# Kernel optimization log

Measured on AMD Instinct MI355X. Metric: run time of the kernel, lower is better.

The kernel has to match this reference:

```python
import jax, jax.numpy as jnp
import numpy as np

N, D = 8192, 1024  # tokens, model dim (d == D required by residual add)


def setup_inputs() -> dict:
    key = jax.random.key(0)
    ks = jax.random.split(key, 6)
    s = 1.0 / np.sqrt(D)
    return {
        "x": jax.random.normal(ks[0], (N, D), dtype=jnp.float32),
        "Wq": jax.random.normal(ks[1], (D, D), dtype=jnp.float32) * s,
        "Wk": jax.random.normal(ks[2], (D, D), dtype=jnp.float32) * s,
        "Wg": jax.random.normal(ks[3], (D, D), dtype=jnp.float32) * s,
        "Wm_w": jax.random.normal(ks[4], (D, 1), dtype=jnp.float32) * s,
        "Wm_b": jnp.zeros((1,), dtype=jnp.float32),
        "c": jnp.asarray(1.0 / np.sqrt(D), dtype=jnp.float32),
    }


def reference(x, Wq, Wk, Wg, Wm_w, Wm_b, c):
    # projections [N, d]
    q_hat = x @ Wq
    k_hat = x @ Wk
    # mean-center over the token axis
    q = q_hat - jnp.mean(q_hat, axis=0, keepdims=True)
    k = k_hat - jnp.mean(k_hat, axis=0, keepdims=True)
    # scaled scores [N, N], row softmax
    attn = jax.nn.softmax(c * (q @ k.T), axis=-1)
    # per-token gate m [N, 1], softmax over tokens, broadcast over columns
    m = x @ Wm_w + Wm_b
    gate = jax.nn.softmax(m, axis=0)
    omega = attn + gate  # [N, N]
    g = x @ Wg           # [N, d]
    return omega @ g + x  # residual, requires d == D
```

## Files before the change

kernel.cpp:

```cpp
#include <hip/hip_runtime.h>
#include <math.h>


#define NT 8192
#define DD 1024

typedef float v4f __attribute__((ext_vector_type(4)));
typedef short v8s __attribute__((ext_vector_type(8)));
typedef int   v4i __attribute__((ext_vector_type(4)));
typedef int   v8i __attribute__((ext_vector_type(8)));

typedef const __attribute__((address_space(1))) void* gp_t;
typedef __attribute__((address_space(3))) void* lp_t;

__device__ __forceinline__ short f2b(float f) {
    unsigned u = __float_as_uint(f);
    return (short)((u + 0x7fffu + ((u >> 16) & 1u)) >> 16);
}
__device__ __forceinline__ char f2e4m3(float f) {
    unsigned p = __builtin_amdgcn_cvt_pk_fp8_f32(f, f, 0, false);
    return (char)(p & 0xff);
}

__device__ __forceinline__ void tile_coords(int bid, int tn, int& bm, int& bn) {
    const int SUP = 16;
    int per = SUP * tn;
    int band = bid / per, r = bid % per;
    bm = band * SUP + (r % SUP);
    bn = r / SUP;
}

__device__ __forceinline__ void gemm_core_fp8(const char* __restrict__ A,
                                              const char* __restrict__ B,
                                              int K, int m0, int n0,
                                              char* smem, v4f (&acc)[4][4])
{
    char* lsA = smem;
    char* lsB = smem + 16384;
    const int tid  = threadIdx.x;
    const int wave = tid >> 6, lane = tid & 63;
    const int l15 = lane & 15, l4 = lane >> 4;
    const int wm = (wave >> 1) << 6, wn = (wave & 1) << 6;

#pragma unroll
    for (int i = 0; i < 4; i++)
#pragma unroll
        for (int j = 0; j < 4; j++) acc[i][j] = (v4f)(0.0f);

    const int srow = lane >> 3;
    const int g    = (lane & 7) ^ srow;

    for (int k0 = 0; k0 < K; k0 += 128) {
#pragma unroll
        for (int i = 0; i < 4; i++) {
            int ci  = wave * 4 + i;
            int row = ci * 8 + srow;
            const char* ga = A + (size_t)(m0 + row) * K + k0 + g * 16;
            const char* gb = B + (size_t)(n0 + row) * K + k0 + g * 16;
            __builtin_amdgcn_global_load_lds((gp_t)ga, (lp_t)(lsA + ci * 1024), 16, 0, 0);
            __builtin_amdgcn_global_load_lds((gp_t)gb, (lp_t)(lsB + ci * 1024), 16, 0, 0);
        }
        __syncthreads();
#pragma unroll
        for (int kk = 0; kk < 128; kk += 32) {
            long af[4], bq[4];
            const int cbase = (kk >> 4) + (l4 >> 1);
            const int half  = (l4 & 1) * 8;
#pragma unroll
            for (int t = 0; t < 4; t++) {
                int ra = wm + t * 16 + l15;
                int ca = cbase ^ (ra & 7);
                af[t] = *(const long*)(lsA + ra * 128 + ca * 16 + half);
                int rb = wn + t * 16 + l15;
                int cb = cbase ^ (rb & 7);
                bq[t] = *(const long*)(lsB + rb * 128 + cb * 16 + half);
            }
#pragma unroll
            for (int i = 0; i < 4; i++)
#pragma unroll
                for (int j = 0; j < 4; j++)
                    acc[i][j] = __builtin_amdgcn_mfma_f32_16x16x32_fp8_fp8(af[i], bq[j], acc[i][j], 0, 0, 0);
        }
        __syncthreads();
    }
}

__device__ __forceinline__ void gemm_core_mx(const char* __restrict__ A,
                                             const char* __restrict__ B,
                                             int K, int m0, int n0,
                                             char* smem, v4f (&acc)[4][4])
{
    char* lsA = smem;
    char* lsB = smem + 16384;
    const int tid  = threadIdx.x;
    const int wave = tid >> 6, lane = tid & 63;
    const int l15 = lane & 15, l4 = lane >> 4;
    const int wm = (wave >> 1) << 6, wn = (wave & 1) << 6;

#pragma unroll
    for (int i = 0; i < 4; i++)
#pragma unroll
        for (int j = 0; j < 4; j++) acc[i][j] = (v4f)(0.0f);

    const int srow = lane >> 3;
    const int g    = (lane & 7) ^ srow;

    for (int k0 = 0; k0 < K; k0 += 128) {
#pragma unroll
        for (int i = 0; i < 4; i++) {
            int ci  = wave * 4 + i;
            int row = ci * 8 + srow;
            const char* ga = A + (size_t)(m0 + row) * K + k0 + g * 16;
            const char* gb = B + (size_t)(n0 + row) * K + k0 + g * 16;
            __builtin_amdgcn_global_load_lds((gp_t)ga, (lp_t)(lsA + ci * 1024), 16, 0, 0);
            __builtin_amdgcn_global_load_lds((gp_t)gb, (lp_t)(lsB + ci * 1024), 16, 0, 0);
        }
        __syncthreads();
        v8i af[4], bq[4];
#pragma unroll
        for (int t = 0; t < 4; t++) {
            int ra = wm + t * 16 + l15;
            int a0 = (2 * l4) ^ (ra & 7), a1 = (2 * l4 + 1) ^ (ra & 7);
            v4i lo = *(const v4i*)(lsA + ra * 128 + a0 * 16);
            v4i hi = *(const v4i*)(lsA + ra * 128 + a1 * 16);
            af[t][0] = lo[0]; af[t][1] = lo[1]; af[t][2] = lo[2]; af[t][3] = lo[3];
            af[t][4] = hi[0]; af[t][5] = hi[1]; af[t][6] = hi[2]; af[t][7] = hi[3];
            int rb = wn + t * 16 + l15;
            int b0 = (2 * l4) ^ (rb & 7), b1 = (2 * l4 + 1) ^ (rb & 7);
            v4i blo = *(const v4i*)(lsB + rb * 128 + b0 * 16);
            v4i bhi = *(const v4i*)(lsB + rb * 128 + b1 * 16);
            bq[t][0] = blo[0]; bq[t][1] = blo[1]; bq[t][2] = blo[2]; bq[t][3] = blo[3];
            bq[t][4] = bhi[0]; bq[t][5] = bhi[1]; bq[t][6] = bhi[2]; bq[t][7] = bhi[3];
        }
#pragma unroll
        for (int i = 0; i < 4; i++)
#pragma unroll
            for (int j = 0; j < 4; j++)
                acc[i][j] = __builtin_amdgcn_mfma_scale_f32_16x16x128_f8f6f4(
                    af[i], bq[j], acc[i][j], 0, 0,
                    0, 0x7f7f7f7f, 0, 0x7f7f7f7f);
        __syncthreads();
    }
}

__global__ void prep(const float* __restrict__ x, const float* __restrict__ wv,
                     const float* __restrict__ bp, char* __restrict__ x8,
                     float* __restrict__ em,
                     const float* __restrict__ Wq, const float* __restrict__ Wk,
                     const float* __restrict__ Wg, char* __restrict__ w8t,
                     float* __restrict__ zero_base) {
    __shared__ float t[64][68];
    int bid = blockIdx.x, tid = threadIdx.x;
    if (bid < 2048) {
        if (bid == 0) {
            for (int i = tid; i < 2 * DD + NT; i += 256) zero_base[i] = 0.f;
        }
        int wv_id = tid >> 6;
        int row = bid * 4 + wv_id;
        int lane = tid & 63;
        const float* xr = x + (size_t)row * DD;
        char* x8r = x8 + (size_t)row * DD;
        float s = 0.f;
        for (int c = lane * 4; c < DD; c += 256) {
            float4 a = *(const float4*)(xr + c);
            float4 b = *(const float4*)(wv + c);
            s = fmaf(a.x, b.x, s); s = fmaf(a.y, b.y, s);
            s = fmaf(a.z, b.z, s); s = fmaf(a.w, b.w, s);
            unsigned p = __builtin_amdgcn_cvt_pk_fp8_f32(a.x, a.y, 0, false);
            p = __builtin_amdgcn_cvt_pk_fp8_f32(a.z, a.w, p, true);
            *(int*)(x8r + c) = (int)p;
        }
        for (int o = 32; o; o >>= 1) s += __shfl_down(s, o);
        if (lane == 0) em[row] = __expf(s + bp[0]);
    } else {
        int idx = bid - 2048;
        int bz = idx >> 8, rem = idx & 255;
        const float* W = bz == 0 ? Wq : (bz == 1 ? Wk : Wg);
        int k0 = (rem & 15) * 64, n0 = (rem >> 4) * 64;
        int tr = tid >> 4, tc = tid & 15;
#pragma unroll
        for (int p = 0; p < 4; p++) {
            int r = p * 16 + tr;
            float4 v = *(const float4*)(W + (size_t)(k0 + r) * DD + n0 + tc * 4);
            t[r][tc * 4 + 0] = v.x; t[r][tc * 4 + 1] = v.y;
            t[r][tc * 4 + 2] = v.z; t[r][tc * 4 + 3] = v.w;
        }
        __syncthreads();
#pragma unroll
        for (int p = 0; p < 4; p++) {
            int rr = p * 16 + tr;
            unsigned pk = __builtin_amdgcn_cvt_pk_fp8_f32(
                16.f * t[tc * 4 + 0][rr], 16.f * t[tc * 4 + 1][rr], 0, false);
            pk = __builtin_amdgcn_cvt_pk_fp8_f32(
                16.f * t[tc * 4 + 2][rr], 16.f * t[tc * 4 + 3][rr], pk, true);
            *(int*)(w8t + (size_t)(bz * DD + n0 + rr) * DD + k0 + tc * 4) = (int)pk;
        }
    }
}

__global__ void beta_gemv(const char* __restrict__ k8, const float* __restrict__ qsum,
                          const float* __restrict__ cp, float* __restrict__ beta,
                          const float* __restrict__ em, float* __restrict__ gden) {
    int tid = threadIdx.x, lane = tid & 63;
    if (blockIdx.x == 2048) {
        __shared__ float sr[4];
        float s = 0.f;
        for (int i = tid; i < NT; i += 256) s += em[i];
        for (int o = 32; o; o >>= 1) s += __shfl_xor(s, o);
        if (lane == 0) sr[tid >> 6] = s;
        __syncthreads();
        if (tid == 0) gden[0] = sr[0] + sr[1] + sr[2] + sr[3];
        return;
    }
    int row = blockIdx.x * 4 + (tid >> 6);
    v4i kv = *(const v4i*)(k8 + (size_t)row * DD + lane * 16);
    const float* qs = qsum + lane * 16;
    float s = 0.f;
#pragma unroll
    for (int w = 0; w < 4; w++) {
        float4 qv = *(const float4*)(qs + w * 4);
        int word = kv[w];
        s = fmaf(__builtin_amdgcn_cvt_f32_fp8(word, 0), qv.x, s);
        s = fmaf(__builtin_amdgcn_cvt_f32_fp8(word, 1), qv.y, s);
        s = fmaf(__builtin_amdgcn_cvt_f32_fp8(word, 2), qv.z, s);
        s = fmaf(__builtin_amdgcn_cvt_f32_fp8(word, 3), qv.w, s);
    }
    for (int o = 32; o; o >>= 1) s += __shfl_down(s, o);
    if (lane == 0) beta[row] = s * cp[0] / (float)NT;
}


__global__ __launch_bounds__(256, 2) void k_proj(
        const char* __restrict__ x8, const char* __restrict__ w8t,
        char* __restrict__ q8, char* __restrict__ k8, char* __restrict__ gbt,
        float* __restrict__ qsum, float* __restrict__ gsum) {
    __shared__ __align__(16) char smem[32768];
    int bm, bn; tile_coords(blockIdx.x, 24, bm, bn);
    int m0 = bm * 128, n0 = bn * 128;
    v4f acc[4][4];
    gemm_core_fp8(x8, w8t, DD, m0, n0, smem, acc);

    const int tid = threadIdx.x, wave = tid >> 6, lane = tid & 63;
    const int l15 = lane & 15, l4 = lane >> 4;
    const int wm = (wave >> 1) << 6, wn = (wave & 1) << 6;
    int sec = n0 >> 10;
    int nloc = n0 & (DD - 1);
    const float WS = 0.0625f;

    if (sec < 2) {
        char* dst = sec ? k8 : q8;
        float cs[4] = {0.f, 0.f, 0.f, 0.f};
#pragma unroll
        for (int i = 0; i < 4; i++)
#pragma unroll
            for (int j = 0; j < 4; j++)
#pragma unroll
                for (int v = 0; v < 4; v++) {
                    int row = m0 + wm + i * 16 + l4 * 4 + v;
                    int col = nloc + wn + j * 16 + l15;
                    float av = acc[i][j][v] * WS;
                    dst[(size_t)row * DD + col] = f2e4m3(av);
                    cs[j] += av;
                }
        if (sec == 0)
#pragma unroll
            for (int j = 0; j < 4; j++)
                atomicAdd(&qsum[nloc + wn + j * 16 + l15], cs[j]);
    } else {
        char* sc = smem;
        float cs[4] = {0.f, 0.f, 0.f, 0.f};
#pragma unroll
        for (int i = 0; i < 4; i++)
#pragma unroll
            for (int j = 0; j < 4; j++)
#pragma unroll
                for (int v = 0; v < 4; v++) {
                    int lr = wn + j * 16 + l15;
                    int lc = wm + i * 16 + l4 * 4 + v;
                    float av = acc[i][j][v] * WS;
                    sc[lr * 144 + lc] = f2e4m3(av);
                    cs[j] += av;
                }
        __syncthreads();
#pragma unroll
        for (int it = 0; it < 4; it++) {
            int c = it * 256 + tid;
            int dr = c >> 3, cm = (c & 7) * 16;
            int4 vv = *(const int4*)(sc + dr * 144 + cm);
            *(int4*)(gbt + (size_t)(nloc + dr) * NT + m0 + cm) = vv;
        }
#pragma unroll
        for (int j = 0; j < 4; j++)
            atomicAdd(&gsum[nloc + wn + j * 16 + l15], cs[j]);
    }
}

__global__ __launch_bounds__(256, 2) void k_score(
        const char* __restrict__ q8, const char* __restrict__ k8,
        char* __restrict__ E, float* __restrict__ l, const float* __restrict__ cptr,
        const float* __restrict__ beta) {
    __shared__ __align__(16) char smem[32768];
    int bm, bn; tile_coords(blockIdx.x, 64, bm, bn);
    int m0 = bm * 128, n0 = bn * 128;
    v4f acc[4][4];
    gemm_core_fp8(q8, k8, DD, m0, n0, smem, acc);

    const float cv = cptr[0];
    const int tid = threadIdx.x, wave = tid >> 6, lane = tid & 63;
    const int l15 = lane & 15, l4 = lane >> 4;
    const int wm = (wave >> 1) << 6, wn = (wave & 1) << 6;
    float bj[4];
#pragma unroll
    for (int j = 0; j < 4; j++) bj[j] = beta[n0 + wn + j * 16 + l15];
#pragma unroll
    for (int i = 0; i < 4; i++)
#pragma unroll
        for (int v = 0; v < 4; v++) {
            int row = m0 + wm + i * 16 + l4 * 4 + v;
            float rsum = 0.f;
#pragma unroll
            for (int j = 0; j < 4; j++) {
                float e = __expf(cv * acc[i][j][v] - bj[j]);
                E[(size_t)row * NT + (n0 + wn + j * 16 + l15)] = f2e4m3(e);
                rsum += e;
            }
#pragma unroll
            for (int o = 1; o < 16; o <<= 1) rsum += __shfl_xor(rsum, o);
            if (l15 == 0) atomicAdd(&l[row], rsum);
        }
}

__global__ __launch_bounds__(256, 2) void k_out(
        const char* __restrict__ E, const char* __restrict__ gbt,
        const float* __restrict__ l, const float* __restrict__ em,
        const float* __restrict__ gden, const float* __restrict__ gsum,
        const float* __restrict__ x, float* __restrict__ out) {
    __shared__ __align__(16) char smem[32768];
    int bm, bn; tile_coords(blockIdx.x, 8, bm, bn);
    int m0 = bm * 128, n0 = bn * 128;
    v4f acc[4][4];
    gemm_core_mx(E, gbt, NT, m0, n0, smem, acc);

    const float ginv = 1.f / gden[0];
    const int tid = threadIdx.x, wave = tid >> 6, lane = tid & 63;
    const int l15 = lane & 15, l4 = lane >> 4;
    const int wm = (wave >> 1) << 6, wn = (wave & 1) << 6;
#pragma unroll
    for (int i = 0; i < 4; i++)
#pragma unroll
        for (int v = 0; v < 4; v++) {
            int row = m0 + wm + i * 16 + l4 * 4 + v;
            float inv = 1.f / l[row];
            float gv  = em[row] * ginv;
#pragma unroll
            for (int j = 0; j < 4; j++) {
                int col = n0 + wn + j * 16 + l15;
                out[(size_t)row * DD + col] =
                    acc[i][j][v] * inv + gv * gsum[col] + x[(size_t)row * DD + col];
            }
        }
}


extern "C" void kernel_launch(void* const* d_in, const int* in_sizes, int n_in,
                              void* d_out, int out_size, void* d_ws, size_t ws_size,
                              hipStream_t stream) {
    const float* x  = (const float*)d_in[0];
    const float* Wq = (const float*)d_in[1];
    const float* Wk = (const float*)d_in[2];
    const float* Wg = (const float*)d_in[3];
    const float* Wm = (const float*)d_in[4];
    const float* Wb = (const float*)d_in[5];
    const float* cp = (const float*)d_in[6];
    float* out = (float*)d_out;

    char* w = (char*)d_ws;
    size_t off = 0;
    auto alloc = [&](size_t bytes) -> void* {
        void* p = w + off;
        off += (bytes + 255) & ~(size_t)255;
        return p;
    };
    char*  q8    = (char*)alloc((size_t)NT * DD);
    char*  k8    = (char*)alloc((size_t)NT * DD);
    char*  gbt   = (char*)alloc((size_t)DD * NT);
    char*  w8t   = (char*)alloc((size_t)3 * DD * DD);
    char*  x8    = (char*)alloc((size_t)NT * DD);
    char*  E     = (char*)alloc((size_t)NT * NT);
    float* stats = (float*)alloc((2 * DD + 3 * NT + 1) * 4);
    float* qsum = stats;
    float* gsum = stats + DD;
    float* lrow = stats + 2 * DD;
    float* gden = lrow + NT;
    float* em   = gden + 1;
    float* beta = em + NT;
    if (off > ws_size) return;

    prep<<<2048 + 768, 256, 0, stream>>>(x, Wm, Wb, x8, em, Wq, Wk, Wg, w8t, stats);
    k_proj<<<64 * 24, 256, 0, stream>>>(x8, w8t, q8, k8, gbt, qsum, gsum);
    beta_gemv<<<2049, 256, 0, stream>>>(k8, qsum, cp, beta, em, gden);
    k_score<<<64 * 64, 256, 0, stream>>>(q8, k8, E, lrow, cp, beta);
    k_out<<<64 * 8, 256, 0, stream>>>(E, gbt, lrow, em, gden, gsum, x, out);
}
```

Measured before the change: 370.3 us.

## Permute fp8 K-layout so GEMM core uses 16-byte LDS fragment reads

Producers of fp8 operands (x8, transposed weights, q8/k8 outputs and qsum) now write columns in a permuted order within each 128-wide K block. The fp8 GEMM core can then load two MFMA K-steps per lane with a single 16-byte LDS read instead of two 8-byte reads, halving LDS read instructions in the inner loop. The permutation must match consistently across all producers and consumers, including later kernels that read q8/k8 and qsum, which is a correctness risk.

```diff
diff --git a/kernel.cpp b/kernel.cpp
--- a/kernel.cpp
+++ b/kernel.cpp
@@ -6,20 +6,19 @@
 #define DD 1024
 
 typedef float v4f __attribute__((ext_vector_type(4)));
-typedef short v8s __attribute__((ext_vector_type(8)));
 typedef int   v4i __attribute__((ext_vector_type(4)));
 typedef int   v8i __attribute__((ext_vector_type(8)));
+typedef long  v2l __attribute__((ext_vector_type(2)));
 
 typedef const __attribute__((address_space(1))) void* gp_t;
 typedef __attribute__((address_space(3))) void* lp_t;
 
-__device__ __forceinline__ short f2b(float f) {
-    unsigned u = __float_as_uint(f);
-    return (short)((u + 0x7fffu + ((u >> 16) & 1u)) >> 16);
-}
 __device__ __forceinline__ char f2e4m3(float f) {
     unsigned p = __builtin_amdgcn_cvt_pk_fp8_f32(f, f, 0, false);
     return (char)(p & 0xff);
+}
+__device__ __forceinline__ int permd(int w) {
+    return ((w >> 6) << 6) | (((w >> 3) & 3) << 4) | (((w >> 5) & 1) << 3) | (w & 7);
 }
 
 __device__ __forceinline__ void tile_coords(int bid, int tn, int& bm, int& bn) {
@@ -62,24 +61,27 @@
         }
         __syncthreads();
 #pragma unroll
-        for (int kk = 0; kk < 128; kk += 32) {
-            long af[4], bq[4];
-            const int cbase = (kk >> 4) + (l4 >> 1);
-            const int half  = (l4 & 1) * 8;
+        for (int p = 0; p < 2; p++) {
+            v2l af[4], bq[4];
 #pragma unroll
             for (int t = 0; t < 4; t++) {
                 int ra = wm + t * 16 + l15;
-                int ca = cbase ^ (ra & 7);
-                af[t] = *(const long*)(lsA + ra * 128 + ca * 16 + half);
+                int ca = (p * 4 + l4) ^ (ra & 7);
+                af[t] = *(const v2l*)(lsA + ra * 128 + ca * 16);
                 int rb = wn + t * 16 + l15;
-                int cb = cbase ^ (rb & 7);
-                bq[t] = *(const long*)(lsB + rb * 128 + cb * 16 + half);
+                int cb = (p * 4 + l4) ^ (rb & 7);
+                bq[t] = *(const v2l*)(lsB + rb * 128 + cb * 16);
             }
 #pragma unroll
             for (int i = 0; i < 4; i++)
 #pragma unroll
                 for (int j = 0; j < 4; j++)
-                    acc[i][j] = __builtin_amdgcn_mfma_f32_16x16x32_fp8_fp8(af[i], bq[j], acc[i][j], 0, 0, 0);
+                    acc[i][j] = __builtin_amdgcn_mfma_f32_16x16x32_fp8_fp8(af[i][0], bq[j][0], acc[i][j], 0, 0, 0);
+#pragma unroll
+            for (int i = 0; i < 4; i++)
+#pragma unroll
+                for (int j = 0; j < 4; j++)
+                    acc[i][j] = __builtin_amdgcn_mfma_f32_16x16x32_fp8_fp8(af[i][1], bq[j][1], acc[i][j], 0, 0, 0);
         }
         __syncthreads();
     }
@@ -168,7 +170,8 @@
             s = fmaf(a.z, b.z, s); s = fmaf(a.w, b.w, s);
             unsigned p = __builtin_amdgcn_cvt_pk_fp8_f32(a.x, a.y, 0, false);
             p = __builtin_amdgcn_cvt_pk_fp8_f32(a.z, a.w, p, true);
-            *(int*)(x8r + c) = (int)p;
+            int cp = (c & ~127) | permd(c & 127);
+            *(int*)(x8r + cp) = (int)p;
         }
         for (int o = 32; o; o >>= 1) s += __shfl_down(s, o);
         if (lane == 0) em[row] = __expf(s + bp[0]);
@@ -193,7 +196,9 @@
                 16.f * t[tc * 4 + 0][rr], 16.f * t[tc * 4 + 1][rr], 0, false);
             pk = __builtin_amdgcn_cvt_pk_fp8_f32(
                 16.f * t[tc * 4 + 2][rr], 16.f * t[tc * 4 + 3][rr], pk, true);
-            *(int*)(w8t + (size_t)(bz * DD + n0 + rr) * DD + k0 + tc * 4) = (int)pk;
+            int kk = k0 + tc * 4;
+            int kp = (kk & ~127) | permd(kk & 127);
+            *(int*)(w8t + (size_t)(bz * DD + n0 + rr) * DD + kp) = (int)pk;
         }
     }
 }
@@ -253,19 +258,20 @@
 #pragma unroll
         for (int i = 0; i < 4; i++)
 #pragma unroll
-            for (int j = 0; j < 4; j++)
+            for (int j = 0; j < 4; j++) {
+                int colp = nloc + permd(wn + j * 16 + l15);
 #pragma unroll
                 for (int v = 0; v < 4; v++) {
                     int row = m0 + wm + i * 16 + l4 * 4 + v;
-                    int col = nloc + wn + j * 16 + l15;
                     float av = acc[i][j][v] * WS;
-                    dst[(size_t)row * DD + col] = f2e4m3(av);
+                    dst[(size_t)row * DD + colp] = f2e4m3(av);
                     cs[j] += av;
                 }
+            }
         if (sec == 0)
 #pragma unroll
             for (int j = 0; j < 4; j++)
-                atomicAdd(&qsum[nloc + wn + j * 16 + l15], cs[j]);
+                atomicAdd(&qsum[nloc + permd(wn + j * 16 + l15)], cs[j]);
     } else {
         char* sc = smem;
         float cs[4] = {0.f, 0.f, 0.f, 0.f};
```

Measured after the change: 367.5 us. No clear change (-0.7%).
